# Kernel tuning notes

Hardware: AMD Instinct MI355X
Metric: run time of the kernel (lower is better)

The kernel has to match this reference:

```python
import jax, jax.numpy as jnp
import numpy as np

B = 1048576
H = 32
DAMP_MIN = jnp.array([0.001, 0.001], dtype=jnp.float32)

def setup_inputs() -> dict:
    key = jax.random.key(0)
    ks = jax.random.split(key, 13)
    u = lambda k, shape: jax.random.uniform(k, shape, jnp.float32, -0.2, 0.2)
    return {
        "x": jax.random.normal(ks[0], (B, 2), jnp.float32),
        "w_d1": u(ks[1], (2, H)),
        "w_d2": u(ks[2], (H, H)),
        "w_d3": u(ks[3], (H, 2)),
        "w_o1": u(ks[4], (2, H)),
        "w_o2": u(ks[5], (H, H)),
        "w_o3": u(ks[6], (H, 1)),
        "b_d1": jnp.zeros((H,), jnp.float32),
        "b_d2": jnp.zeros((H,), jnp.float32),
        "b_d3": jnp.zeros((2,), jnp.float32),
        "b_o1": jnp.zeros((H,), jnp.float32),
        "b_o2": jnp.zeros((H,), jnp.float32),
        "b_o3": jnp.zeros((1,), jnp.float32),
    }

def reference(x, w_d1, w_d2, w_d3, w_o1, w_o2, w_o3,
              b_d1, b_d2, b_d3, b_o1, b_o2, b_o3):
    # diag branch: 2-layer tanh MLP -> relu, scaled by x
    d1t = jnp.tanh(x @ w_d1 + b_d1)
    d2t = jnp.tanh(d1t @ w_d2 + b_d2)
    d3 = d2t @ w_d3 + b_d3                       # [B,2]
    d3r = (jax.nn.relu(d3) + DAMP_MIN) * x       # diag of L, [B,2]
    # off-diag branch -> single lower-triangular element per sample
    o1t = jnp.tanh(x @ w_o1 + b_o1)
    o2t = jnp.tanh(o1t @ w_o2 + b_o2)
    o3 = o2t @ w_o3 + b_o3                       # [B,1]
    # L = [[a,0],[c,b]] per sample; D = (L L^T) x, vectorized over batch.
    a = d3r[:, 0]
    b = d3r[:, 1]
    c = o3[:, 0]
    x0 = x[:, 0]
    x1 = x[:, 1]
    D0 = a * a * x0 + a * c * x1
    D1 = a * c * x0 + (c * c + b * b) * x1
    return jnp.stack([D0, D1], axis=-1)          # [B,2]
```

## Files before the change

kernel.cpp:

```cpp
#include <hip/hip_runtime.h>


typedef __bf16 bf16x8 __attribute__((ext_vector_type(8)));
typedef float f32x4 __attribute__((ext_vector_type(4)));
typedef int i32x4 __attribute__((ext_vector_type(4)));

__device__ __forceinline__ float fast_tanh(float x) {
    float e = __builtin_amdgcn_exp2f(x * 2.8853900817779268f);
    float r = __builtin_amdgcn_rcpf(e + 1.0f);
    return __builtin_fmaf(-2.0f, r, 1.0f);
}

__device__ __forceinline__ int pack_bf16(float f0, float f1) {
    unsigned u0 = __builtin_bit_cast(unsigned, f0) + 0x8000u;
    unsigned u1 = __builtin_bit_cast(unsigned, f1) + 0x8000u;
    return (int)__builtin_amdgcn_perm(u1, u0, 0x07060302u);
}

__global__ __launch_bounds__(256, 3) void damping_mfma(
    const float* __restrict__ x,
    const float* __restrict__ w_d1, const float* __restrict__ w_d2, const float* __restrict__ w_d3,
    const float* __restrict__ w_o1, const float* __restrict__ w_o2, const float* __restrict__ w_o3,
    const float* __restrict__ b_d1, const float* __restrict__ b_d2, const float* __restrict__ b_d3,
    const float* __restrict__ b_o1, const float* __restrict__ b_o2, const float* __restrict__ b_o3,
    float* __restrict__ out, int n_tiles)
{
    const int lane = threadIdx.x & 63;
    const int quad = lane >> 4;
    const int b16  = lane & 15;
    const int wid     = (int)((blockIdx.x * blockDim.x + threadIdx.x) >> 6);
    const int n_waves = (int)((gridDim.x * blockDim.x) >> 6);

    float w1d0[8], w1d1[8], bd1[8], w1o0[8], w1o1[8], bo1[8];
    #pragma unroll
    for (int j = 0; j < 8; ++j) {
        int k = quad * 8 + j;
        w1d0[j] = w_d1[k]; w1d1[j] = w_d1[32 + k]; bd1[j] = b_d1[k];
        w1o0[j] = w_o1[k]; w1o1[j] = w_o1[32 + k]; bo1[j] = b_o1[k];
    }
    bf16x8 a_d2[2], a_o2[2];
    #pragma unroll
    for (int t = 0; t < 2; ++t) {
        #pragma unroll
        for (int j = 0; j < 8; ++j) {
            int k = quad * 8 + j;
            a_d2[t][j] = (__bf16)w_d2[k * 32 + t * 16 + b16];
            a_o2[t][j] = (__bf16)w_o2[k * 32 + t * 16 + b16];
        }
    }
    float bd2[8], bo2[8], w3d0[8], w3d1[8], w3o[8];
    #pragma unroll
    for (int i = 0; i < 8; ++i) {
        int jj = (i >> 2) * 16 + quad * 4 + (i & 3);
        bd2[i]  = b_d2[jj]; bo2[i] = b_o2[jj];
        w3d0[i] = w_d3[jj * 2]; w3d1[i] = w_d3[jj * 2 + 1];
        w3o[i]  = w_o3[jj];
    }
    const float bd3_0 = b_d3[0], bd3_1 = b_d3[1], bo3_0 = b_o3[0];

    const float2* x2 = (const float2*)x;
    int tile = wid;
    if (tile >= n_tiles) return;
    float2 xv = x2[tile * 16 + b16];

    for (; tile < n_tiles; tile += n_waves) {
        int nt = tile + n_waves;
        nt = (nt < n_tiles) ? nt : tile;
        float2 xnext = x2[nt * 16 + b16];

        const float x0 = xv.x, x1 = xv.y;

        float hd[8], ho[8];
        #pragma unroll
        for (int j = 0; j < 8; ++j) {
            hd[j] = fast_tanh(fmaf(x1, w1d1[j], fmaf(x0, w1d0[j], bd1[j])));
            ho[j] = fast_tanh(fmaf(x1, w1o1[j], fmaf(x0, w1o0[j], bo1[j])));
        }
        i32x4 pd_, po_;
        #pragma unroll
        for (int p = 0; p < 4; ++p) {
            pd_[p] = pack_bf16(hd[2 * p], hd[2 * p + 1]);
            po_[p] = pack_bf16(ho[2 * p], ho[2 * p + 1]);
        }
        bf16x8 bfd = __builtin_bit_cast(bf16x8, pd_);
        bf16x8 bfo = __builtin_bit_cast(bf16x8, po_);

        f32x4 zero = {0.f, 0.f, 0.f, 0.f};
        f32x4 d0 = __builtin_amdgcn_mfma_f32_16x16x32_bf16(a_d2[0], bfd, zero, 0, 0, 0);
        f32x4 d1 = __builtin_amdgcn_mfma_f32_16x16x32_bf16(a_d2[1], bfd, zero, 0, 0, 0);
        f32x4 o0 = __builtin_amdgcn_mfma_f32_16x16x32_bf16(a_o2[0], bfo, zero, 0, 0, 0);
        f32x4 o1 = __builtin_amdgcn_mfma_f32_16x16x32_bf16(a_o2[1], bfo, zero, 0, 0, 0);

        float pd0 = 0.f, pd1 = 0.f, po = 0.f;
        #pragma unroll
        for (int i = 0; i < 8; ++i) {
            float vd = (i < 4 ? d0[i] : d1[i - 4]) + bd2[i];
            float vo = (i < 4 ? o0[i] : o1[i - 4]) + bo2[i];
            float h2d = fast_tanh(vd);
            float h2o = fast_tanh(vo);
            pd0 = fmaf(h2d, w3d0[i], pd0);
            pd1 = fmaf(h2d, w3d1[i], pd1);
            po  = fmaf(h2o, w3o[i], po);
        }
        pd0 += __shfl_xor(pd0, 16); pd0 += __shfl_xor(pd0, 32);
        pd1 += __shfl_xor(pd1, 16); pd1 += __shfl_xor(pd1, 32);
        po  += __shfl_xor(po, 16);  po  += __shfl_xor(po, 32);

        float d30 = pd0 + bd3_0, d31 = pd1 + bd3_1, c = po + bo3_0;
        float a = (fmaxf(d30, 0.f) + 0.001f) * x0;
        float b = (fmaxf(d31, 0.f) + 0.001f) * x1;
        float D0 = fmaf(a * a, x0, a * c * x1);
        float D1 = fmaf(a * c, x0, fmaf(c, c, b * b) * x1);

        if (quad == 0) ((float2*)out)[tile * 16 + b16] = make_float2(D0, D1);
        xv = xnext;
    }
}

extern "C" void kernel_launch(void* const* d_in, const int* in_sizes, int n_in,
                              void* d_out, int out_size, void* d_ws, size_t ws_size,
                              hipStream_t stream) {
    const float* x    = (const float*)d_in[0];
    const float* w_d1 = (const float*)d_in[1];
    const float* w_d2 = (const float*)d_in[2];
    const float* w_d3 = (const float*)d_in[3];
    const float* w_o1 = (const float*)d_in[4];
    const float* w_o2 = (const float*)d_in[5];
    const float* w_o3 = (const float*)d_in[6];
    const float* b_d1 = (const float*)d_in[7];
    const float* b_d2 = (const float*)d_in[8];
    const float* b_d3 = (const float*)d_in[9];
    const float* b_o1 = (const float*)d_in[10];
    const float* b_o2 = (const float*)d_in[11];
    const float* b_o3 = (const float*)d_in[12];
    float* out = (float*)d_out;

    int n = in_sizes[0] / 2;
    int n_tiles = n / 16;
    int blocks_needed = (n_tiles + 3) / 4;
    int grid = blocks_needed < 768 ? blocks_needed : 768;
    damping_mfma<<<grid, 256, 0, stream>>>(
        x, w_d1, w_d2, w_d3, w_o1, w_o2, w_o3,
        b_d1, b_d2, b_d3, b_o1, b_o2, b_o3, out, n_tiles);
}
```

Before: 126.5 us.

## Fold tanh scale into weights, seed MFMA with bias, use permlane swaps

Pre-multiplies the first- and second-layer weights and biases by the tanh exp2 constant, so each tanh skips one multiply. The second-layer bias is passed as the MFMA accumulator instead of being added afterwards. The xor-shuffle reductions become v_permlane16/32_swap sequences. Launch bounds go to 8 waves per EU and the grid cap rises to 2048 blocks. Other changes: bf16 packing now uses compiler casts instead of manual round-and-perm, and scaling the bf16 weights slightly changes rounding.

```diff
diff --git a/kernel.cpp b/kernel.cpp
--- a/kernel.cpp
+++ b/kernel.cpp
@@ -3,21 +3,25 @@
 
 typedef __bf16 bf16x8 __attribute__((ext_vector_type(8)));
 typedef float f32x4 __attribute__((ext_vector_type(4)));
-typedef int i32x4 __attribute__((ext_vector_type(4)));
 
-__device__ __forceinline__ float fast_tanh(float x) {
-    float e = __builtin_amdgcn_exp2f(x * 2.8853900817779268f);
+#define KTANH 2.8853900817779268f
+
+__device__ __forceinline__ float tanh_pre(float z) {
+    float e = __builtin_amdgcn_exp2f(z);
     float r = __builtin_amdgcn_rcpf(e + 1.0f);
     return __builtin_fmaf(-2.0f, r, 1.0f);
 }
 
-__device__ __forceinline__ int pack_bf16(float f0, float f1) {
-    unsigned u0 = __builtin_bit_cast(unsigned, f0) + 0x8000u;
-    unsigned u1 = __builtin_bit_cast(unsigned, f1) + 0x8000u;
-    return (int)__builtin_amdgcn_perm(u1, u0, 0x07060302u);
+__device__ __forceinline__ float quad_sum(float v) {
+    float a = v, b = v;
+    asm("v_permlane16_swap_b32 %0, %1" : "+v"(a), "+v"(b));
+    float s = a + b;
+    float c = s, d = s;
+    asm("v_permlane32_swap_b32 %0, %1" : "+v"(c), "+v"(d));
+    return c + d;
 }
 
-__global__ __launch_bounds__(256, 3) void damping_mfma(
+__global__ __launch_bounds__(256, 8) void damping_mfma(
     const float* __restrict__ x,
     const float* __restrict__ w_d1, const float* __restrict__ w_d2, const float* __restrict__ w_d3,
     const float* __restrict__ w_o1, const float* __restrict__ w_o2, const float* __restrict__ w_o3,
@@ -35,8 +39,8 @@
     #pragma unroll
     for (int j = 0; j < 8; ++j) {
         int k = quad * 8 + j;
-        w1d0[j] = w_d1[k]; w1d1[j] = w_d1[32 + k]; bd1[j] = b_d1[k];
-        w1o0[j] = w_o1[k]; w1o1[j] = w_o1[32 + k]; bo1[j] = b_o1[k];
+        w1d0[j] = w_d1[k] * KTANH; w1d1[j] = w_d1[32 + k] * KTANH; bd1[j] = b_d1[k] * KTANH;
+        w1o0[j] = w_o1[k] * KTANH; w1o1[j] = w_o1[32 + k] * KTANH; bo1[j] = b_o1[k] * KTANH;
     }
     bf16x8 a_d2[2], a_o2[2];
     #pragma unroll
@@ -44,15 +48,24 @@
         #pragma unroll
         for (int j = 0; j < 8; ++j) {
             int k = quad * 8 + j;
-            a_d2[t][j] = (__bf16)w_d2[k * 32 + t * 16 + b16];
-            a_o2[t][j] = (__bf16)w_o2[k * 32 + t * 16 + b16];
+            a_d2[t][j] = (__bf16)(w_d2[k * 32 + t * 16 + b16] * KTANH);
+            a_o2[t][j] = (__bf16)(w_o2[k * 32 + t * 16 + b16] * KTANH);
         }
     }
-    float bd2[8], bo2[8], w3d0[8], w3d1[8], w3o[8];
+    f32x4 cd[2], co[2];
+    #pragma unroll
+    for (int t = 0; t < 2; ++t) {
+        #pragma unroll
+        for (int i = 0; i < 4; ++i) {
+            int jj = t * 16 + quad * 4 + i;
+            cd[t][i] = b_d2[jj] * KTANH;
+            co[t][i] = b_o2[jj] * KTANH;
+        }
+    }
+    float w3d0[8], w3d1[8], w3o[8];
     #pragma unroll
     for (int i = 0; i < 8; ++i) {
         int jj = (i >> 2) * 16 + quad * 4 + (i & 3);
-        bd2[i]  = b_d2[jj]; bo2[i] = b_o2[jj];
         w3d0[i] = w_d3[jj * 2]; w3d1[i] = w_d3[jj * 2 + 1];
         w3o[i]  = w_o3[jj];
     }
@@ -73,38 +86,33 @@
         float hd[8], ho[8];
         #pragma unroll
         for (int j = 0; j < 8; ++j) {
-            hd[j] = fast_tanh(fmaf(x1, w1d1[j], fmaf(x0, w1d0[j], bd1[j])));
-            ho[j] = fast_tanh(fmaf(x1, w1o1[j], fmaf(x0, w1o0[j], bo1[j])));
+            hd[j] = tanh_pre(fmaf(x1, w1d1[j], fmaf(x0, w1d0[j], bd1[j])));
+            ho[j] = tanh_pre(fmaf(x1, w1o1[j], fmaf(x0, w1o0[j], bo1[j])));
         }
-        i32x4 pd_, po_;
+        bf16x8 bfd, bfo;
         #pragma unroll
-        for (int p = 0; p < 4; ++p) {
-            pd_[p] = pack_bf16(hd[2 * p], hd[2 * p + 1]);
-            po_[p] = pack_bf16(ho[2 * p], ho[2 * p + 1]);
+        for (int j = 0; j < 8; ++j) {
+            bfd[j] = (__bf16)hd[j];
+            bfo[j] = (__bf16)ho[j];
         }
-        bf16x8 bfd = __builtin_bit_cast(bf16x8, pd_);
-        bf16x8 bfo = __builtin_bit_cast(bf16x8, po_);
 
-        f32x4 zero = {0.f, 0.f, 0.f, 0.f};
-        f32x4 d0 = __builtin_amdgcn_mfma_f32_16x16x32_bf16(a_d2[0], bfd, zero, 0, 0, 0);
-        f32x4 d1 = __builtin_amdgcn_mfma_f32_16x16x32_bf16(a_d2[1], bfd, zero, 0, 0, 0);
-        f32x4 o0 = __builtin_amdgcn_mfma_f32_16x16x32_bf16(a_o2[0], bfo, zero, 0, 0, 0);
-        f32x4 o1 = __builtin_amdgcn_mfma_f32_16x16x32_bf16(a_o2[1], bfo, zero, 0, 0, 0);
+        f32x4 d0 = __builtin_amdgcn_mfma_f32_16x16x32_bf16(a_d2[0], bfd, cd[0], 0, 0, 0);
+        f32x4 d1 = __builtin_amdgcn_mfma_f32_16x16x32_bf16(a_d2[1], bfd, cd[1], 0, 0, 0);
+        f32x4 o0 = __builtin_amdgcn_mfma_f32_16x16x32_bf16(a_o2[0], bfo, co[0], 0, 0, 0);
+        f32x4 o1 = __builtin_amdgcn_mfma_f32_16x16x32_bf16(a_o2[1], bfo, co[1], 0, 0, 0);
 
         float pd0 = 0.f, pd1 = 0.f, po = 0.f;
         #pragma unroll
         for (int i = 0; i < 8; ++i) {
-            float vd = (i < 4 ? d0[i] : d1[i - 4]) + bd2[i];
-            float vo = (i < 4 ? o0[i] : o1[i - 4]) + bo2[i];
-            float h2d = fast_tanh(vd);
-            float h2o = fast_tanh(vo);
+            float h2d = tanh_pre(i < 4 ? d0[i] : d1[i - 4]);
+            float h2o = tanh_pre(i < 4 ? o0[i] : o1[i - 4]);
             pd0 = fmaf(h2d, w3d0[i], pd0);
             pd1 = fmaf(h2d, w3d1[i], pd1);
             po  = fmaf(h2o, w3o[i], po);
         }
-        pd0 += __shfl_xor(pd0, 16); pd0 += __shfl_xor(pd0, 32);
-        pd1 += __shfl_xor(pd1, 16); pd1 += __shfl_xor(pd1, 32);
-        po  += __shfl_xor(po, 16);  po  += __shfl_xor(po, 32);
+        pd0 = quad_sum(pd0);
+        pd1 = quad_sum(pd1);
+        po  = quad_sum(po);
 
         float d30 = pd0 + bd3_0, d31 = pd1 + bd3_1, c = po + bo3_0;
         float a = (fmaxf(d30, 0.f) + 0.001f) * x0;
@@ -138,7 +146,7 @@
     int n = in_sizes[0] / 2;
     int n_tiles = n / 16;
     int blocks_needed = (n_tiles + 3) / 4;
-    int grid = blocks_needed < 768 ? blocks_needed : 768;
+    int grid = blocks_needed < 2048 ? blocks_needed : 2048;
     damping_mfma<<<grid, 256, 0, stream>>>(
         x, w_d1, w_d2, w_d3, w_o1, w_o2, w_o3,
         b_d1, b_d2, b_d3, b_o1, b_o2, b_o3, out, n_tiles);
```

After: 268.4 us. +112.2%, slower.
